# Optimization experiments

Measured on AMD Instinct MI355X. Metric: run time of the kernel, lower is better.

Reference implementation:

```python
import jax, jax.numpy as jnp
import numpy as np
from jax import lax

D_MODEL = 512
NUM_HEADS = 8
HEADDIM = D_MODEL // NUM_HEADS      # 64
EXPAND = 2
D_INNER = EXPAND * D_MODEL          # 1024
D_STATE = 64
NGROUPS = 1
KCONV = 4                           # window_size -> depthwise conv kernel
NHEADS = D_INNER // HEADDIM         # 16 SSM heads
D_FF = 2048
CONV_DIM = D_INNER + 2 * NGROUPS * D_STATE          # 1152 (x, B, C)
D_IN_PROJ = 2 * D_INNER + 2 * NGROUPS * D_STATE + NHEADS  # 2192 (z, x, B, C, dt)
EPS = 1e-6


def _rmsnorm(x, eps=EPS):
    return x * lax.rsqrt(jnp.mean(x * x, axis=-1, keepdims=True) + eps)


def _silu(x):
    return x * jax.nn.sigmoid(x)


def _ssm_scan(xs, dt, A, Bm, Cm):
    # xs: [B,L,H,P], dt: [B,L,H], A: [H], Bm/Cm: [B,L,N]  (ngroups=1 broadcast over heads)
    dA = jnp.exp(dt * A)                 # [B,L,H] decay per step
    dBx = dt[..., None] * xs             # [B,L,H,P] input contribution
    h0 = jnp.zeros((xs.shape[0], xs.shape[2], xs.shape[3], Bm.shape[2]), xs.dtype)

    def step(h, t):
        dA_t, dBx_t, B_t, C_t = t        # [B,H],[B,H,P],[B,N],[B,N]
        h = dA_t[..., None, None] * h + dBx_t[..., None] * B_t[:, None, None, :]
        y = jnp.einsum('bhpn,bn->bhp', h, C_t)
        return h, y

    _, ys = lax.scan(step, h0, (dA.transpose(1, 0, 2), dBx.transpose(1, 0, 2, 3),
                                Bm.transpose(1, 0, 2), Cm.transpose(1, 0, 2)))
    return ys.transpose(1, 0, 2, 3)      # [B,L,H,P]


def setup_inputs() -> dict:
    key = jax.random.key(0)
    ks = jax.random.split(key, 12)
    B, L = 8, 2048
    s = 0.02
    inp = {
        'x': jax.random.normal(ks[0], (B, L, D_MODEL), jnp.float32),
        'mask': jnp.ones((B, L), jnp.float32),
        'W_in': jax.random.normal(ks[1], (D_MODEL, D_IN_PROJ), jnp.float32) * s,
        'conv_w': jax.random.normal(ks[2], (CONV_DIM, KCONV), jnp.float32) * 0.1,
        'conv_b': jnp.zeros((CONV_DIM,), jnp.float32),
        'dt_bias': jax.random.normal(ks[3], (NHEADS,), jnp.float32) * 0.1,
        'A_log': jnp.log(jnp.arange(1, NHEADS + 1, dtype=jnp.float32)),
        'D': jnp.ones((NHEADS,), jnp.float32),
        'norm_w': jnp.ones((D_INNER,), jnp.float32),
        'W_out': jax.random.normal(ks[4], (D_INNER, D_MODEL), jnp.float32) * s,
        'W1': jax.random.normal(ks[5], (D_MODEL, D_FF), jnp.float32) * s,
        'b1': jnp.zeros((D_FF,), jnp.float32),
        'W2': jax.random.normal(ks[6], (D_FF, D_MODEL), jnp.float32) * s,
        'b2': jnp.zeros((D_MODEL,), jnp.float32),
    }
    return inp


def reference(x, mask, W_in, conv_w, conv_b, dt_bias, A_log, D, norm_w, W_out, W1, b1, W2, b2):
    B, L, _ = x.shape
    x = x * mask[..., None]
    u = _rmsnorm(x)

    zxbcdt = u @ W_in                                   # [B,L,2192]
    z = zxbcdt[..., :D_INNER]
    xBC = zxbcdt[..., D_INNER:D_INNER + CONV_DIM]
    dt = zxbcdt[..., D_INNER + CONV_DIM:]               # [B,L,H]

    # causal depthwise conv1d, kernel KCONV
    pad = jnp.pad(xBC, ((0, 0), (KCONV - 1, 0), (0, 0)))
    xBC = sum(pad[:, i:i + L, :] * conv_w[:, i] for i in range(KCONV)) + conv_b
    xBC = _silu(xBC) * mask[..., None]

    xs = xBC[..., :D_INNER].reshape(B, L, NHEADS, HEADDIM)
    Bm = xBC[..., D_INNER:D_INNER + D_STATE]            # [B,L,N] (ngroups=1)
    Cm = xBC[..., D_INNER + D_STATE:]

    dt = jax.nn.softplus(dt + dt_bias)
    A = -jnp.exp(A_log)                                 # [H]

    # bidirectional (non-causal) selective scan: forward + reversed scans
    y_f = _ssm_scan(xs, dt, A, Bm, Cm)
    y_b = _ssm_scan(xs[:, ::-1], dt[:, ::-1], A, Bm[:, ::-1], Cm[:, ::-1])[:, ::-1]
    y = y_f + y_b + D[None, None, :, None] * xs         # [B,L,H,P]
    y = y.reshape(B, L, D_INNER)

    # gated RMSNorm then output projection
    y = _rmsnorm(y * _silu(z)) * norm_w
    m = y @ W_out                                       # mamba2 output, [B,L,D]

    x = m + m                                           # x = x + dropout1(x) with x := mamba out
    h = _rmsnorm(x)
    x = x + (jax.nn.gelu(h @ W1 + b1) @ W2 + b2)        # x + mlp(norm2(x))
    return (x, m, dt, z)
```

## Files before the change

### kernel.cpp

```cpp
#include <hip/hip_runtime.h>
#include <cstdint>
#include <cstddef>

#define L_SEQ   2048
#define NROWS   16384
#define D_MODEL 512
#define D_INNER 1024
#define D_STATE 64
#define NHEADS  16
#define CONV_DIM 1152
#define D_IN_PROJ 2192
#define D_FF 2048
#define EPS 1e-6f

typedef __bf16 bf16_t;
typedef __bf16 bf16x8 __attribute__((ext_vector_type(8)));
typedef __bf16 bf16x4 __attribute__((ext_vector_type(4)));
typedef float  f32x4  __attribute__((ext_vector_type(4)));

#define OFF_WT_IN    0ull
#define OFF_WT_OUT   2244608ull
#define OFF_W1T      3293184ull
#define OFF_W2T      5390336ull
#define OFF_U        7487488ull
#define OFF_XBC_RAW  24264704ull
#define OFF_XBC_CONV 99762176ull
#define OFF_Y2       175259648ull
#define OFF_YN       242368512ull

__device__ __forceinline__ void gl_lds16(const void* g, void* s) {
  __builtin_amdgcn_global_load_lds(
      (__attribute__((address_space(1))) void*)(void*)g,
      (__attribute__((address_space(3))) void*)s, 16, 0, 0);
}

__device__ __forceinline__ float block_sum256(float v, float* red) {
#pragma unroll
  for (int o = 32; o > 0; o >>= 1) v += __shfl_xor(v, o, 64);
  int w = threadIdx.x >> 6;
  if ((threadIdx.x & 63) == 0) red[w] = v;
  __syncthreads();
  return red[0] + red[1] + red[2] + red[3];
}

__device__ __forceinline__ float softplus_f(float x) {
  return (x > 20.f) ? x : log1pf(expf(x));
}
__device__ __forceinline__ float silu_f(float x) {
  return x / (1.f + expf(-x));
}
__device__ __forceinline__ float gelu_tanh_f(float x) {
  float x3 = x * x * x;
  return 0.5f * x * (1.f + tanhf(0.7978845608f * (x + 0.044715f * x3)));
}

__global__ __launch_bounds__(256) void prep_weights_kernel(
    const float* __restrict__ W_in, const float* __restrict__ W_out,
    const float* __restrict__ W1, const float* __restrict__ W2,
    bf16_t* __restrict__ wt_in, bf16_t* __restrict__ wt_out,
    bf16_t* __restrict__ w1t, bf16_t* __restrict__ w2t) {
  const int S1 = D_IN_PROJ * 512;
  const int S2 = 512 * 1024;
  const int S3 = 2048 * 512;
  const int S4 = 512 * 2048;
  const int total = S1 + S2 + S3 + S4;
  for (int i = blockIdx.x * 256 + threadIdx.x; i < total; i += gridDim.x * 256) {
    if (i < S1) {
      int n = i / 512, k = i - n * 512;
      wt_in[i] = (bf16_t)W_in[k * D_IN_PROJ + n];
    } else if (i < S1 + S2) {
      int j = i - S1; int n = j >> 10, k = j & 1023;
      wt_out[j] = (bf16_t)W_out[k * 512 + n];
    } else if (i < S1 + S2 + S3) {
      int j = i - S1 - S2; int n = j >> 9, k = j & 511;
      w1t[j] = (bf16_t)W1[k * 2048 + n];
    } else {
      int j = i - S1 - S2 - S3; int n = j >> 11, k = j & 2047;
      w2t[j] = (bf16_t)W2[k * 512 + n];
    }
  }
}

__global__ __launch_bounds__(256) void rmsnorm_in_kernel(
    const float* __restrict__ x, const float* __restrict__ mask,
    bf16_t* __restrict__ u) {
  __shared__ float red[4];
  int row = blockIdx.x;
  float mk = mask[row];
  const float* xr = x + (size_t)row * 512;
  float v0 = xr[threadIdx.x] * mk;
  float v1 = xr[threadIdx.x + 256] * mk;
  float ss = block_sum256(v0 * v0 + v1 * v1, red);
  float r = rsqrtf(ss * (1.f / 512.f) + EPS);
  bf16_t* ur = u + (size_t)row * 512;
  ur[threadIdx.x] = (bf16_t)(v0 * r);
  ur[threadIdx.x + 256] = (bf16_t)(v1 * r);
}

__global__ __launch_bounds__(256) void rmsnorm2_kernel(
    const float* __restrict__ m, bf16_t* __restrict__ h) {
  __shared__ float red[4];
  int row = blockIdx.x;
  const float* mr = m + (size_t)row * 512;
  float v0 = 2.f * mr[threadIdx.x];
  float v1 = 2.f * mr[threadIdx.x + 256];
  float ss = block_sum256(v0 * v0 + v1 * v1, red);
  float r = rsqrtf(ss * (1.f / 512.f) + EPS);
  bf16_t* hr = h + (size_t)row * 512;
  hr[threadIdx.x] = (bf16_t)(v0 * r);
  hr[threadIdx.x + 256] = (bf16_t)(v1 * r);
}

template <int EPI>
__global__ __launch_bounds__(256, 2) void gemm_kernel(
    const bf16_t* __restrict__ A, const bf16_t* __restrict__ Bt,
    int M, int N, int K,
    float* __restrict__ o0, float* __restrict__ o1, float* __restrict__ o2,
    bf16_t* __restrict__ ob, const float* __restrict__ bias,
    const float* __restrict__ extra) {
  __shared__ bf16_t As[2][128 * 32];
  __shared__ bf16_t Bs[2][128 * 32];
  const int tid = threadIdx.x;
  const int lane = tid & 63;
  const int w = tid >> 6;
  const int tileM = blockIdx.y * 128;
  const int tileN = blockIdx.x * 128;

  f32x4 acc[4][4] = {};

  const int wm = (w >> 1) * 64;
  const int wn = (w & 1) * 64;
  const int fr = lane & 15;
  const int fk = (lane >> 4) * 8;

  const int rsub = lane >> 2;
  const int cb   = (lane & 3) * 16;

  auto stage = [&](int buf, int k0) {
#pragma unroll
    for (int i = 0; i < 2; ++i) {
      int rloc = w * 32 + i * 16 + rsub;
      const char* ga = (const char*)(A + (size_t)(tileM + rloc) * K + k0) + cb;
      gl_lds16(ga, (void*)&As[buf][(w * 32 + i * 16) * 32]);
      int rn = tileN + rloc;
      if (rn >= N) rn = N - 1;
      const char* gb = (const char*)(Bt + (size_t)rn * K + k0) + cb;
      gl_lds16(gb, (void*)&Bs[buf][(w * 32 + i * 16) * 32]);
    }
  };

  const int nt = K >> 5;
  stage(0, 0);
  __syncthreads();
  int cur = 0;
  for (int t = 0; t < nt; ++t) {
    if (t + 1 < nt) stage(cur ^ 1, (t + 1) << 5);

    bf16x8 av[4], bv[4];
#pragma unroll
    for (int i = 0; i < 4; ++i)
      av[i] = *(const bf16x8*)&As[cur][(wm + i * 16 + fr) * 32 + fk];
#pragma unroll
    for (int j = 0; j < 4; ++j)
      bv[j] = *(const bf16x8*)&Bs[cur][(wn + j * 16 + fr) * 32 + fk];
#pragma unroll
    for (int i = 0; i < 4; ++i)
#pragma unroll
      for (int j = 0; j < 4; ++j)
        acc[i][j] = __builtin_amdgcn_mfma_f32_16x16x32_bf16(av[i], bv[j], acc[i][j], 0, 0, 0);

    __syncthreads();
    cur ^= 1;
  }

  const int cn = lane & 15;
  const int r0 = (lane >> 4) * 4;
#pragma unroll
  for (int i = 0; i < 4; ++i) {
#pragma unroll
    for (int j = 0; j < 4; ++j) {
      int gn = tileN + wn + j * 16 + cn;
      if (gn >= N) continue;
#pragma unroll
      for (int r = 0; r < 4; ++r) {
        int gm = tileM + wm + i * 16 + r0 + r;
        float v = acc[i][j][r];
        if (EPI == 0) {
          o0[(size_t)gm * N + gn] = v;
        } else if (EPI == 1) {
          if (gn < D_INNER) {
            o0[(size_t)gm * D_INNER + gn] = v;
          } else if (gn < D_INNER + CONV_DIM) {
            o1[(size_t)gm * CONV_DIM + (gn - D_INNER)] = v;
          } else {
            int hh = gn - (D_INNER + CONV_DIM);
            o2[(size_t)gm * NHEADS + hh] = softplus_f(v + bias[hh]);
          }
        } else if (EPI == 2) {
          ob[(size_t)gm * N + gn] = (bf16_t)gelu_tanh_f(v + bias[gn]);
        } else if (EPI == 3) {
          o0[(size_t)gm * N + gn] = v + bias[gn] + 2.f * extra[(size_t)gm * N + gn];
        }
      }
    }
  }
}

__global__ __launch_bounds__(320) void conv_silu_kernel(
    const float* __restrict__ xbc_raw, const float* __restrict__ conv_w,
    const float* __restrict__ conv_b, const float* __restrict__ mask,
    bf16_t* __restrict__ xbc_conv) {
  int row = blockIdx.x;
  int tid = threadIdx.x;
  if (tid >= 288) return;
  int t = row & (L_SEQ - 1);
  float mk = mask[row];
  int c = tid * 4;
  const float* base = xbc_raw + (size_t)row * CONV_DIM + c;
  float4 z4 = {0.f, 0.f, 0.f, 0.f};
  float4 r0 = *(const float4*)base;
  float4 r1 = (t >= 1) ? *(const float4*)(base - CONV_DIM) : z4;
  float4 r2 = (t >= 2) ? *(const float4*)(base - 2 * CONV_DIM) : z4;
  float4 r3 = (t >= 3) ? *(const float4*)(base - 3 * CONV_DIM) : z4;
  const float* p0 = (const float*)&r0;
  const float* p1 = (const float*)&r1;
  const float* p2 = (const float*)&r2;
  const float* p3 = (const float*)&r3;
  bf16x4 o;
#pragma unroll
  for (int j = 0; j < 4; ++j) {
    float4 wv = ((const float4*)conv_w)[c + j];
    float acc = conv_b[c + j] + wv.x * p3[j] + wv.y * p2[j] + wv.z * p1[j] + wv.w * p0[j];
    o[j] = (bf16_t)(silu_f(acc) * mk);
  }
  *(bf16x4*)&xbc_conv[(size_t)row * CONV_DIM + c] = o;
}


__global__ __launch_bounds__(256) void scan_chunk_kernel(
    const bf16_t* __restrict__ xbc, const float* __restrict__ dt_all,
    const float* __restrict__ A_log,
    bf16_t* __restrict__ y2, bf16_t* __restrict__ Tc_buf,
    float* __restrict__ la_buf) {
  const int bid = blockIdx.x;
  const int c = bid & 31, h = (bid >> 5) & 15, b = (bid >> 9) & 7, dir = bid >> 12;
  const float A_h = -expf(A_log[h]);
  const int tid = threadIdx.x, w = tid >> 6, lane = tid & 63;
  const int fr = lane & 15, fk = (lane >> 4) * 8;

  __shared__ __align__(16) bf16_t sB[64][72];
  __shared__ __align__(16) bf16_t sC[64][72];
  __shared__ __align__(16) bf16_t sXt[64][72];
  __shared__ __align__(16) bf16_t sBwt[64][72];
  __shared__ float sLa[64], sDt[64], sW[64];

  const size_t base = (size_t)b * L_SEQ;
#define ROWOF(i) (base + (size_t)(dir ? (L_SEQ - 1 - (c * 64 + (i))) : (c * 64 + (i))))

  if (tid < 64) sDt[tid] = dt_all[ROWOF(tid) * NHEADS + h];

  float bB[16];
#pragma unroll
  for (int r = 0; r < 16; ++r) {
    int i = w * 16 + r;
    const bf16_t* src = xbc + ROWOF(i) * CONV_DIM;
    bf16_t xv = src[h * 64 + lane];
    bf16_t bv = src[D_INNER + lane];
    bf16_t cv = src[D_INNER + D_STATE + lane];
    bB[r] = (float)bv;
    sB[i][lane] = bv;
    sC[i][lane] = cv;
    sXt[lane][i] = xv;
  }
  __syncthreads();

  if (w == 0) {
    float v = sDt[lane] * A_h;
#pragma unroll
    for (int d = 1; d < 64; d <<= 1) {
      float o = __shfl_up(v, d, 64);
      if (lane >= d) v += o;
    }
    sLa[lane] = v;
    float la63 = __shfl(v, 63, 64);
    sW[lane] = __expf(la63 - v) * sDt[lane];
  }
  __syncthreads();

#pragma unroll
  for (int r = 0; r < 16; ++r) {
    int i = w * 16 + r;
    sBwt[lane][i] = (bf16_t)(bB[r] * sW[i]);
  }
  if (tid < 64) la_buf[(size_t)bid * 64 + tid] = sLa[tid];

  f32x4 acc1[4] = {};
#pragma unroll
  for (int k0 = 0; k0 < 64; k0 += 32) {
    bf16x8 bv = *(const bf16x8*)&sC[w * 16 + fr][k0 + fk];
#pragma unroll
    for (int mi = 0; mi < 4; ++mi) {
      if (mi <= w) {
        bf16x8 av = *(const bf16x8*)&sB[mi * 16 + fr][k0 + fk];
        acc1[mi] = __builtin_amdgcn_mfma_f32_16x16x32_bf16(av, bv, acc1[mi], 0, 0, 0);
      }
    }
  }
  __syncthreads();

  {
    bf16_t (*sM)[72] = sB;
    float la_t = sLa[w * 16 + fr];
    int t = w * 16 + fr;
#pragma unroll
    for (int mi = 0; mi < 4; ++mi) {
#pragma unroll
      for (int r = 0; r < 4; ++r) {
        int s = mi * 16 + (lane >> 4) * 4 + r;
        float mv = 0.f;
        if (s <= t) mv = acc1[mi][r] * __expf(la_t - sLa[s]) * sDt[s];
        sM[t][s] = (bf16_t)mv;
      }
    }
  }

  f32x4 acc3[4] = {};
#pragma unroll
  for (int k0 = 0; k0 < 64; k0 += 32) {
    bf16x8 bv = *(const bf16x8*)&sBwt[w * 16 + fr][k0 + fk];
#pragma unroll
    for (int mi = 0; mi < 4; ++mi) {
      bf16x8 av = *(const bf16x8*)&sXt[mi * 16 + fr][k0 + fk];
      acc3[mi] = __builtin_amdgcn_mfma_f32_16x16x32_bf16(av, bv, acc3[mi], 0, 0, 0);
    }
  }
  __syncthreads();

  f32x4 acc2[4] = {};
  {
    bf16_t (*sM)[72] = sB;
#pragma unroll
    for (int k0 = 0; k0 < 64; k0 += 32) {
      bf16x8 bv = *(const bf16x8*)&sXt[w * 16 + fr][k0 + fk];
#pragma unroll
      for (int mi = 0; mi < 4; ++mi) {
        bf16x8 av = *(const bf16x8*)&sM[mi * 16 + fr][k0 + fk];
        acc2[mi] = __builtin_amdgcn_mfma_f32_16x16x32_bf16(av, bv, acc2[mi], 0, 0, 0);
      }
    }
  }

  bf16_t* yout = y2 + (size_t)dir * NROWS * D_INNER;
  bf16_t* tco = Tc_buf + (size_t)bid * 4096;
#pragma unroll
  for (int mi = 0; mi < 4; ++mi) {
#pragma unroll
    for (int r = 0; r < 4; ++r) {
      int rowl = mi * 16 + (lane >> 4) * 4 + r;
      int coll = w * 16 + fr;
      yout[ROWOF(rowl) * D_INNER + h * 64 + coll] = (bf16_t)acc2[mi][r];
      tco[rowl * 64 + coll] = (bf16_t)acc3[mi][r];
    }
  }
#undef ROWOF
}

__global__ __launch_bounds__(256) void state_prefix_kernel(
    const float* __restrict__ la_buf, bf16_t* __restrict__ Tc_buf) {
  const int g = blockIdx.x >> 1;
  const int e0 = (blockIdx.x & 1) * 2048 + threadIdx.x * 8;
  bf16_t* tc = Tc_buf + (size_t)g * 32 * 4096 + e0;
  const float* la63 = la_buf + (size_t)g * 32 * 64 + 63;
  float S[8] = {};
  for (int cc = 0; cc < 32; ++cc) {
    bf16x8 t = *(const bf16x8*)(tc + (size_t)cc * 4096);
    float d = __expf(la63[cc * 64]);
    bf16_t sb[8];
#pragma unroll
    for (int j = 0; j < 8; ++j) sb[j] = (bf16_t)S[j];
    *(bf16x8*)(tc + (size_t)cc * 4096) = *(bf16x8*)sb;
    const bf16_t* tp = (const bf16_t*)&t;
#pragma unroll
    for (int j = 0; j < 8; ++j) S[j] = d * S[j] + (float)tp[j];
  }
}

__global__ __launch_bounds__(256) void ystate_kernel(
    const bf16_t* __restrict__ xbc, const bf16_t* __restrict__ S_buf,
    const float* __restrict__ la_buf, bf16_t* __restrict__ y2) {
  const int bid = blockIdx.x;
  const int hg = bid & 3, c = (bid >> 2) & 31, b = (bid >> 7) & 7, dir = bid >> 10;
  const int tid = threadIdx.x, w = tid >> 6, lane = tid & 63;
  const int fr = lane & 15, fk = (lane >> 4) * 8;
  const size_t base = (size_t)b * L_SEQ;

  __shared__ __align__(16) bf16_t sC[64][72];
  __shared__ __align__(16) float  sYf[64][72];
  __shared__ float sEla[64];

#pragma unroll
  for (int uu = 0; uu < 2; ++uu) {
    int u = tid + uu * 256;
    int row = u >> 3, q = u & 7;
    int t = c * 64 + row;
    int tr = dir ? (L_SEQ - 1 - t) : t;
    bf16x8 cv = *(const bf16x8*)(xbc + (base + tr) * CONV_DIM + D_INNER + D_STATE + q * 8);
    *(bf16x8*)&sC[row][q * 8] = cv;
  }
  __syncthreads();

  bf16_t* yout = y2 + (size_t)dir * NROWS * D_INNER;

#pragma unroll 1
  for (int hi = 0; hi < 4; ++hi) {
    const int h = hg * 4 + hi;
    const int bidh = dir * 4096 + b * 512 + h * 32 + c;
    if (tid < 64) sEla[tid] = __expf(la_buf[(size_t)bidh * 64 + tid]);

    const bf16_t* Sp = S_buf + (size_t)bidh * 4096;
    f32x4 acc[4] = {};
#pragma unroll
    for (int k0 = 0; k0 < 64; k0 += 32) {
      bf16x8 bv = *(const bf16x8*)(Sp + (w * 16 + fr) * 64 + k0 + fk);
#pragma unroll
      for (int mi = 0; mi < 4; ++mi) {
        bf16x8 av = *(const bf16x8*)&sC[mi * 16 + fr][k0 + fk];
        acc[mi] = __builtin_amdgcn_mfma_f32_16x16x32_bf16(av, bv, acc[mi], 0, 0, 0);
      }
    }
    __syncthreads();

#pragma unroll
    for (int mi = 0; mi < 4; ++mi) {
#pragma unroll
      for (int r = 0; r < 4; ++r) {
        int tl = mi * 16 + (lane >> 4) * 4 + r;
        sYf[tl][w * 16 + fr] = acc[mi][r] * sEla[tl];
      }
    }
    __syncthreads();

#pragma unroll
    for (int uu = 0; uu < 2; ++uu) {
      int u = tid + uu * 256;
      int row = u >> 3, oct = u & 7;
      int t = c * 64 + row;
      int tr = dir ? (L_SEQ - 1 - t) : t;
      bf16_t* gp = yout + (base + tr) * D_INNER + h * 64 + oct * 8;
      bf16x8 old = *(const bf16x8*)gp;
      const float* yp = &sYf[row][oct * 8];
      bf16x8 nw;
#pragma unroll
      for (int j = 0; j < 8; ++j) nw[j] = (bf16_t)((float)old[j] + yp[j]);
      *(bf16x8*)gp = nw;
    }
  }
}

__global__ __launch_bounds__(256) void combine_kernel(
    const bf16_t* __restrict__ y2, const bf16_t* __restrict__ xbc_conv,
    const float* __restrict__ z, const float* __restrict__ Dp,
    const float* __restrict__ norm_w, bf16_t* __restrict__ yn) {
  __shared__ float red[4];
  int row = blockIdx.x;
  int c0 = threadIdx.x * 4;
  const bf16_t* yf = y2 + (size_t)row * D_INNER;
  const bf16_t* yb = y2 + (size_t)NROWS * D_INNER + (size_t)row * D_INNER;
  const bf16_t* xs = xbc_conv + (size_t)row * CONV_DIM;
  const float* zr = z + (size_t)row * D_INNER;

  bf16x4 vf = *(const bf16x4*)&yf[c0];
  bf16x4 vb = *(const bf16x4*)&yb[c0];
  bf16x4 vx = *(const bf16x4*)&xs[c0];
  f32x4 vz = *(const f32x4*)&zr[c0];
  float Dh = Dp[c0 >> 6];

  float g[4];
  float ss = 0.f;
#pragma unroll
  for (int j = 0; j < 4; ++j) {
    float v = (float)vf[j] + (float)vb[j] + Dh * (float)vx[j];
    float gg = v * silu_f(vz[j]);
    g[j] = gg;
    ss += gg * gg;
  }
  ss = block_sum256(ss, red);
  float r = rsqrtf(ss * (1.f / 1024.f) + EPS);
  bf16x4 o;
#pragma unroll
  for (int j = 0; j < 4; ++j) o[j] = (bf16_t)(g[j] * r * norm_w[c0 + j]);
  *(bf16x4*)&yn[(size_t)row * D_INNER + c0] = o;
}

extern "C" void kernel_launch(void* const* d_in, const int* in_sizes, int n_in,
                              void* d_out, int out_size, void* d_ws, size_t ws_size,
                              hipStream_t stream) {
  const float* x       = (const float*)d_in[0];
  const float* mask    = (const float*)d_in[1];
  const float* W_in    = (const float*)d_in[2];
  const float* conv_w  = (const float*)d_in[3];
  const float* conv_b  = (const float*)d_in[4];
  const float* dt_bias = (const float*)d_in[5];
  const float* A_log   = (const float*)d_in[6];
  const float* Dp      = (const float*)d_in[7];
  const float* norm_w  = (const float*)d_in[8];
  const float* W_out   = (const float*)d_in[9];
  const float* W1      = (const float*)d_in[10];
  const float* b1      = (const float*)d_in[11];
  const float* W2      = (const float*)d_in[12];
  const float* b2      = (const float*)d_in[13];

  float* out_x  = (float*)d_out;
  float* out_m  = out_x + (size_t)NROWS * 512;
  float* out_dt = out_m + (size_t)NROWS * 512;
  float* out_z  = out_dt + (size_t)NROWS * NHEADS;

  char* ws = (char*)d_ws;
  bf16_t* wt_in    = (bf16_t*)(ws + OFF_WT_IN);
  bf16_t* wt_out   = (bf16_t*)(ws + OFF_WT_OUT);
  bf16_t* w1t      = (bf16_t*)(ws + OFF_W1T);
  bf16_t* w2t      = (bf16_t*)(ws + OFF_W2T);
  bf16_t* u_bf     = (bf16_t*)(ws + OFF_U);
  float*  xbc_raw  = (float*)(ws + OFF_XBC_RAW);
  bf16_t* xbc_conv = (bf16_t*)(ws + OFF_XBC_CONV);
  bf16_t* y2       = (bf16_t*)(ws + OFF_Y2);
  bf16_t* yn       = (bf16_t*)(ws + OFF_YN);
  bf16_t* h_bf     = u_bf;
  bf16_t* gelu_bf  = (bf16_t*)(ws + OFF_XBC_RAW);
  bf16_t* Tc_buf   = (bf16_t*)(ws + OFF_XBC_RAW);
  float*  la_buf   = (float*)(ws + OFF_U);

  prep_weights_kernel<<<14624, 256, 0, stream>>>(W_in, W_out, W1, W2, wt_in, wt_out, w1t, w2t);
  rmsnorm_in_kernel<<<NROWS, 256, 0, stream>>>(x, mask, u_bf);
  gemm_kernel<1><<<dim3(18, 128), 256, 0, stream>>>(u_bf, wt_in, NROWS, D_IN_PROJ, 512,
                                                    out_z, xbc_raw, out_dt, nullptr, dt_bias, nullptr);
  conv_silu_kernel<<<NROWS, 320, 0, stream>>>(xbc_raw, conv_w, conv_b, mask, xbc_conv);
  scan_chunk_kernel<<<8192, 256, 0, stream>>>(xbc_conv, out_dt, A_log, y2, Tc_buf, la_buf);
  state_prefix_kernel<<<512, 256, 0, stream>>>(la_buf, Tc_buf);
  ystate_kernel<<<2048, 256, 0, stream>>>(xbc_conv, Tc_buf, la_buf, y2);
  combine_kernel<<<NROWS, 256, 0, stream>>>(y2, xbc_conv, out_z, Dp, norm_w, yn);
  gemm_kernel<0><<<dim3(4, 128), 256, 0, stream>>>(yn, wt_out, NROWS, 512, 1024,
                                                   out_m, nullptr, nullptr, nullptr, nullptr, nullptr);
  rmsnorm2_kernel<<<NROWS, 256, 0, stream>>>(out_m, h_bf);
  gemm_kernel<2><<<dim3(16, 128), 256, 0, stream>>>(h_bf, w1t, NROWS, D_FF, 512,
                                                    nullptr, nullptr, nullptr, gelu_bf, b1, nullptr);
  gemm_kernel<3><<<dim3(4, 128), 256, 0, stream>>>(gelu_bf, w2t, NROWS, 512, D_FF,
                                                   out_x, nullptr, nullptr, nullptr, b2, out_m);
}
```

Measured before the change: 663.4 us.

## Tile weight transposes, store xBC in bf16, raise GEMM occupancy hint

Replaces the strided single-kernel weight transpose-cast with a shared-memory 32x32 tiled transpose launched once per weight matrix, so both reads and writes are coalesced. The in-projection GEMM now writes the xBC slice as bf16 instead of fp32, which halves the write and the conv kernel's read traffic for that intermediate. The GEMM launch bounds hint changes from 2 to 4 blocks per CU, which may force register spilling. Rounding xBC to bf16 before the conv adds a small precision loss.

```diff
diff --git a/kernel.cpp b/kernel.cpp
--- a/kernel.cpp
+++ b/kernel.cpp
@@ -54,30 +54,25 @@
   return 0.5f * x * (1.f + tanhf(0.7978845608f * (x + 0.044715f * x3)));
 }
 
-__global__ __launch_bounds__(256) void prep_weights_kernel(
-    const float* __restrict__ W_in, const float* __restrict__ W_out,
-    const float* __restrict__ W1, const float* __restrict__ W2,
-    bf16_t* __restrict__ wt_in, bf16_t* __restrict__ wt_out,
-    bf16_t* __restrict__ w1t, bf16_t* __restrict__ w2t) {
-  const int S1 = D_IN_PROJ * 512;
-  const int S2 = 512 * 1024;
-  const int S3 = 2048 * 512;
-  const int S4 = 512 * 2048;
-  const int total = S1 + S2 + S3 + S4;
-  for (int i = blockIdx.x * 256 + threadIdx.x; i < total; i += gridDim.x * 256) {
-    if (i < S1) {
-      int n = i / 512, k = i - n * 512;
-      wt_in[i] = (bf16_t)W_in[k * D_IN_PROJ + n];
-    } else if (i < S1 + S2) {
-      int j = i - S1; int n = j >> 10, k = j & 1023;
-      wt_out[j] = (bf16_t)W_out[k * 512 + n];
-    } else if (i < S1 + S2 + S3) {
-      int j = i - S1 - S2; int n = j >> 9, k = j & 511;
-      w1t[j] = (bf16_t)W1[k * 2048 + n];
-    } else {
-      int j = i - S1 - S2 - S3; int n = j >> 11, k = j & 2047;
-      w2t[j] = (bf16_t)W2[k * 512 + n];
-    }
+__global__ __launch_bounds__(256) void transpose_cast_kernel(
+    const float* __restrict__ src, bf16_t* __restrict__ dst, int R, int C) {
+  __shared__ float tile[32][33];
+  const int tx = threadIdx.x & 31;
+  const int ty = threadIdx.x >> 5;
+  const int r0 = blockIdx.y * 32;
+  const int c0 = blockIdx.x * 32;
+#pragma unroll
+  for (int j = 0; j < 4; ++j) {
+    int r = r0 + ty + j * 8;
+    int c = c0 + tx;
+    if (r < R && c < C) tile[ty + j * 8][tx] = src[(size_t)r * C + c];
+  }
+  __syncthreads();
+#pragma unroll
+  for (int j = 0; j < 4; ++j) {
+    int c = c0 + ty + j * 8;
+    int r = r0 + tx;
+    if (c < C && r < R) dst[(size_t)c * R + r] = (bf16_t)tile[tx][ty + j * 8];
   }
 }
 
@@ -112,7 +107,7 @@
 }
 
 template <int EPI>
-__global__ __launch_bounds__(256, 2) void gemm_kernel(
+__global__ __launch_bounds__(256, 4) void gemm_kernel(
     const bf16_t* __restrict__ A, const bf16_t* __restrict__ Bt,
     int M, int N, int K,
     float* __restrict__ o0, float* __restrict__ o1, float* __restrict__ o2,
@@ -191,7 +186,7 @@
           if (gn < D_INNER) {
             o0[(size_t)gm * D_INNER + gn] = v;
           } else if (gn < D_INNER + CONV_DIM) {
-            o1[(size_t)gm * CONV_DIM + (gn - D_INNER)] = v;
+            ob[(size_t)gm * CONV_DIM + (gn - D_INNER)] = (bf16_t)v;
           } else {
             int hh = gn - (D_INNER + CONV_DIM);
             o2[(size_t)gm * NHEADS + hh] = softplus_f(v + bias[hh]);
@@ -207,7 +202,7 @@
 }
 
 __global__ __launch_bounds__(320) void conv_silu_kernel(
-    const float* __restrict__ xbc_raw, const float* __restrict__ conv_w,
+    const bf16_t* __restrict__ xbc_raw, const float* __restrict__ conv_w,
     const float* __restrict__ conv_b, const float* __restrict__ mask,
     bf16_t* __restrict__ xbc_conv) {
   int row = blockIdx.x;
@@ -216,21 +211,18 @@
   int t = row & (L_SEQ - 1);
   float mk = mask[row];
   int c = tid * 4;
-  const float* base = xbc_raw + (size_t)row * CONV_DIM + c;
-  float4 z4 = {0.f, 0.f, 0.f, 0.f};
-  float4 r0 = *(const float4*)base;
-  float4 r1 = (t >= 1) ? *(const float4*)(base - CONV_DIM) : z4;
-  float4 r2 = (t >= 2) ? *(const float4*)(base - 2 * CONV_DIM) : z4;
-  float4 r3 = (t >= 3) ? *(const float4*)(base - 3 * CONV_DIM) : z4;
-  const float* p0 = (const float*)&r0;
-  const float* p1 = (const float*)&r1;
-  const float* p2 = (const float*)&r2;
-  const float* p3 = (const float*)&r3;
+  const bf16_t* base = xbc_raw + (size_t)row * CONV_DIM + c;
+  bf16x4 z4 = {};
+  bf16x4 r0 = *(const bf16x4*)base;
+  bf16x4 r1 = (t >= 1) ? *(const bf16x4*)(base - CONV_DIM) : z4;
+  bf16x4 r2 = (t >= 2) ? *(const bf16x4*)(base - 2 * CONV_DIM) : z4;
+  bf16x4 r3 = (t >= 3) ? *(const bf16x4*)(base - 3 * CONV_DIM) : z4;
   bf16x4 o;
 #pragma unroll
   for (int j = 0; j < 4; ++j) {
     float4 wv = ((const float4*)conv_w)[c + j];
-    float acc = conv_b[c + j] + wv.x * p3[j] + wv.y * p2[j] + wv.z * p1[j] + wv.w * p0[j];
+    float acc = conv_b[c + j] + wv.x * (float)r3[j] + wv.y * (float)r2[j] +
+                wv.z * (float)r1[j] + wv.w * (float)r0[j];
     o[j] = (bf16_t)(silu_f(acc) * mk);
   }
   *(bf16x4*)&xbc_conv[(size_t)row * CONV_DIM + c] = o;
@@ -521,7 +513,7 @@
   bf16_t* w1t      = (bf16_t*)(ws + OFF_W1T);
   bf16_t* w2t      = (bf16_t*)(ws + OFF_W2T);
   bf16_t* u_bf     = (bf16_t*)(ws + OFF_U);
-  float*  xbc_raw  = (float*)(ws + OFF_XBC_RAW);
+  bf16_t* xbc_bf   = (bf16_t*)(ws + OFF_XBC_RAW);
   bf16_t* xbc_conv = (bf16_t*)(ws + OFF_XBC_CONV);
   bf16_t* y2       = (bf16_t*)(ws + OFF_Y2);
   bf16_t* yn       = (bf16_t*)(ws + OFF_YN);
@@ -530,11 +522,14 @@
   bf16_t* Tc_buf   = (bf16_t*)(ws + OFF_XBC_RAW);
   float*  la_buf   = (float*)(ws + OFF_U);
 
-  prep_weights_kernel<<<14624, 256, 0, stream>>>(W_in, W_out, W1, W2, wt_in, wt_out, w1t, w2t);
+  transpose_cast_kernel<<<dim3(69, 16), 256, 0, stream>>>(W_in, wt_in, 512, D_IN_PROJ);
+  transpose_cast_kernel<<<dim3(16, 32), 256, 0, stream>>>(W_out, wt_out, 1024, 512);
+  transpose_cast_kernel<<<dim3(64, 16), 256, 0, stream>>>(W1, w1t, 512, 2048);
+  transpose_cast_kernel<<<dim3(16, 64), 256, 0, stream>>>(W2, w2t, 2048, 512);
   rmsnorm_in_kernel<<<NROWS, 256, 0, stream>>>(x, mask, u_bf);
   gemm_kernel<1><<<dim3(18, 128), 256, 0, stream>>>(u_bf, wt_in, NROWS, D_IN_PROJ, 512,
-                                                    out_z, xbc_raw, out_dt, nullptr, dt_bias, nullptr);
-  conv_silu_kernel<<<NROWS, 320, 0, stream>>>(xbc_raw, conv_w, conv_b, mask, xbc_conv);
+                                                    out_z, nullptr, out_dt, xbc_bf, dt_bias, nullptr);
+  conv_silu_kernel<<<NROWS, 320, 0, stream>>>(xbc_bf, conv_w, conv_b, mask, xbc_conv);
   scan_chunk_kernel<<<8192, 256, 0, stream>>>(xbc_conv, out_dt, A_log, y2, Tc_buf, la_buf);
   state_prefix_kernel<<<512, 256, 0, stream>>>(la_buf, Tc_buf);
   ystate_kernel<<<2048, 256, 0, stream>>>(xbc_conv, Tc_buf, la_buf, y2);
```

Result: faster. 624.5 us (-5.9%).
